# Performance work log

Measured on AMD Instinct MI355X. Metric: run time of the kernel, lower is better.

Reference implementation:

```python
import jax, jax.numpy as jnp
import numpy as np

GRID_SIZE = 5
SPLINE_ORDER = 3
NUM_BASIS = GRID_SIZE + SPLINE_ORDER  # 8


def make_grid():
    # knots: grid_size + 2*spline_order + 1 = 12 points over extended [-1,1]
    h = 2.0 / GRID_SIZE
    return (jnp.arange(-SPLINE_ORDER, GRID_SIZE + SPLINE_ORDER + 1, dtype=jnp.float32) * h - 1.0)[None, :]  # (1, 12)


def b_splines(x, grid):
    # x: (N, in) -> bases: (N, in, NUM_BASIS) via Cox-de Boor recursion
    x = x[..., None]  # (N, in, 1)
    bases = ((x >= grid[:, :-1]) & (x < grid[:, 1:])).astype(x.dtype)
    for p in range(1, SPLINE_ORDER + 1):
        left = (x - grid[:, : -(p + 1)]) / (grid[:, p:-1] - grid[:, : -(p + 1)])
        right = (grid[:, p + 1:] - x) / (grid[:, p + 1:] - grid[:, 1:-p])
        bases = left * bases[..., :-1] + right * bases[..., 1:]
    return bases


def kan_linear(x, base_w, spline_w, scaler, grid):
    # x: (N, in); base_w: (out, in); spline_w: (out, in, G); scaler: (out, in)
    base = jnp.einsum('ni,oi->no', jax.nn.silu(x), base_w)
    bases = b_splines(x, grid)  # (N, in, G)
    spline = jnp.einsum('nig,oig->no', bases, spline_w * scaler[..., None])
    return base + spline


def setup_inputs() -> dict:
    key = jax.random.key(0)
    ks = jax.random.split(key, 7)
    H, L = 768, 2
    hidden = jax.random.normal(ks[0], (32, 512, H), dtype=jnp.float32)
    s = 0.1
    return {
        'hidden': hidden,
        'base_w1': jax.random.normal(ks[1], (H, H), jnp.float32) * s,
        'spline_w1': jax.random.normal(ks[2], (H, H, NUM_BASIS), jnp.float32) * s,
        'scaler1': jax.random.normal(ks[3], (H, H), jnp.float32) * s + 1.0,
        'base_w2': jax.random.normal(ks[4], (L, H), jnp.float32) * s,
        'spline_w2': jax.random.normal(ks[5], (L, H, NUM_BASIS), jnp.float32) * s,
        'scaler2': jax.random.normal(ks[6], (L, H), jnp.float32) * s + 1.0,
    }


def reference(hidden, base_w1, spline_w1, scaler1, base_w2, spline_w2, scaler2):
    grid = make_grid()
    B, S, H = hidden.shape
    x = hidden.reshape(-1, H)  # (N, H)
    x = kan_linear(x, base_w1, spline_w1, scaler1, grid)
    x = jax.nn.gelu(x, approximate=False)  # torch F.gelu default = erf
    out = kan_linear(x, base_w2, spline_w2, scaler2, grid)  # (N, L)
    return out.reshape(B, S, -1).squeeze(-1) if out.shape[-1] == 1 else out.reshape(B, S, -1)
```

## Files before the change

kernel.cpp:

```cpp
#include <hip/hip_runtime.h>
#include <math.h>

#define NROWS 16384
#define H     768
#define KEXP  6912
#define NCHUNK 108
#define NITER 54

typedef __attribute__((ext_vector_type(8))) short  bhalf8;
typedef __attribute__((ext_vector_type(4))) float  floatx4;

__device__ __forceinline__ unsigned short f2bf(float f) {
    unsigned int u = __float_as_uint(f);
    u = (u + 0x7FFFu + ((u >> 16) & 1u)) >> 16;
    return (unsigned short)u;
}
__device__ __forceinline__ float bf2f(unsigned short h) {
    return __uint_as_float(((unsigned int)h) << 16);
}
__device__ __forceinline__ unsigned int pack2(unsigned short a, unsigned short b) {
    return (unsigned int)a | ((unsigned int)b << 16);
}
__device__ __forceinline__ float silu_f(float x) { return x / (1.0f + __expf(-x)); }

__device__ __forceinline__ float gelu_fast(float x) {
    float x3 = x * x * x;
    float y = fmaf(x3, 0.0356774081f, x * 0.7978845608f);
    float e = __expf(2.0f * y);
    float th = 1.0f - 2.0f / (e + 1.0f);
    return 0.5f * x * (1.0f + th);
}

__device__ __forceinline__ void kan_bases(float x, float* __restrict__ b) {
    const float c6 = 0.166666666667f;
    float u  = fmaf(x, 2.5f, 5.5f);
    float fj = floorf(u);
    float t  = u - fj;
    int  j0  = (int)fj;
    float t2 = t * t, t3 = t2 * t;
    float n0 = t3 * c6;
    float n1 = fmaf(t3, -0.5f, fmaf(t2, 0.5f, fmaf(t, 0.5f, c6)));
    float n2 = fmaf(t3, 0.5f, fmaf(t2, -1.0f, 0.666666666667f));
    float omt = 1.0f - t;
    float n3 = omt * omt * omt * c6;
#pragma unroll
    for (int c = 0; c < 8; ++c) {
        int d = j0 - c;
        float v = (d == 0) ? n0 : 0.0f;
        v = (d == 1) ? n1 : v;
        v = (d == 2) ? n2 : v;
        v = (d == 3) ? n3 : v;
        b[c] = v;
    }
}

__global__ __launch_bounds__(256) void prep_expand(
    const float* __restrict__ x, const float* __restrict__ bw,
    const float* __restrict__ sw, const float* __restrict__ sc,
    unsigned short* __restrict__ wp, unsigned short* __restrict__ F)
{
    const int b = blockIdx.x, t = threadIdx.x;
    if (b < 6144) {
        const int e0 = b * 2048 + t;
#pragma unroll
        for (int j = 0; j < 8; ++j) {
            int e = e0 + j * 256;
            int n = e / 768;
            int i = e - n * 768;
            float xv = x[e];
            unsigned short* out = F + (size_t)n * KEXP;
            out[i] = f2bf(silu_f(xv));
            float bb[8];
            kan_bases(xv, bb);
            uint4 pk;
            pk.x = pack2(f2bf(bb[0]), f2bf(bb[1]));
            pk.y = pack2(f2bf(bb[2]), f2bf(bb[3]));
            pk.z = pack2(f2bf(bb[4]), f2bf(bb[5]));
            pk.w = pack2(f2bf(bb[6]), f2bf(bb[7]));
            *(uint4*)(out + H + (size_t)i * 8) = pk;
        }
    } else {
        const int n = b - 6144;
        const float* bwr = bw + (size_t)n * H;
        unsigned short* out = wp + (size_t)n * KEXP;
        if (t < 96) {
            const float4* xp = (const float4*)(bwr + t * 8);
            float4 v0 = xp[0], v1 = xp[1];
            uint4 pk;
            pk.x = pack2(f2bf(v0.x), f2bf(v0.y));
            pk.y = pack2(f2bf(v0.z), f2bf(v0.w));
            pk.z = pack2(f2bf(v1.x), f2bf(v1.y));
            pk.w = pack2(f2bf(v1.z), f2bf(v1.w));
            *(uint4*)(out + t * 8) = pk;
        }
#pragma unroll
        for (int p = 0; p < 3; ++p) {
            int i = t + p * 256;
            float s = sc[(size_t)n * H + i];
            const float4* swp = (const float4*)(sw + ((size_t)n * H + i) * 8);
            float4 w0 = swp[0], w1 = swp[1];
            uint4 pk;
            pk.x = pack2(f2bf(w0.x * s), f2bf(w0.y * s));
            pk.y = pack2(f2bf(w0.z * s), f2bf(w0.w * s));
            pk.z = pack2(f2bf(w1.x * s), f2bf(w1.y * s));
            pk.w = pack2(f2bf(w1.z * s), f2bf(w1.w * s));
            *(uint4*)(out + H + (size_t)i * 8) = pk;
        }
    }
}


#define AS1 __attribute__((address_space(1)))
#define AS3 __attribute__((address_space(3)))

#define DSR(D, A, O) asm volatile("ds_read_b128 %0, %1 offset:" #O : "=v"(D) : "v"(A) : "memory")
#define LDA0(O) do{ DSR(fA0[0],avA[0],O); DSR(fA0[1],avA[1],O); DSR(fA0[2],avA[2],O); DSR(fA0[3],avA[3],O); \
                    DSR(fA0[4],avA[4],O); DSR(fA0[5],avA[5],O); DSR(fA0[6],avA[6],O); DSR(fA0[7],avA[7],O); }while(0)
#define LDA1(O) do{ DSR(fA1[0],avA[0],O); DSR(fA1[1],avA[1],O); DSR(fA1[2],avA[2],O); DSR(fA1[3],avA[3],O); \
                    DSR(fA1[4],avA[4],O); DSR(fA1[5],avA[5],O); DSR(fA1[6],avA[6],O); DSR(fA1[7],avA[7],O); }while(0)
#define LDB(O)  do{ DSR(fB[0],avB[0],O); DSR(fB[1],avB[1],O); }while(0)

#define MM0(QN) do{ \
    _Pragma("unroll") \
    for (int kk = 0; kk < 2; ++kk) \
        _Pragma("unroll") \
        for (int im = 0; im < 4; ++im) \
            acc0[QN][im] = __builtin_amdgcn_mfma_f32_16x16x32_bf16( \
                fA0[im*2+kk], fB[kk], acc0[QN][im], 0, 0, 0); \
}while(0)
#define MM1(QN) do{ \
    _Pragma("unroll") \
    for (int kk = 0; kk < 2; ++kk) \
        _Pragma("unroll") \
        for (int im = 0; im < 4; ++im) \
            acc1[QN][im] = __builtin_amdgcn_mfma_f32_16x16x32_bf16( \
                fA1[im*2+kk], fB[kk], acc1[QN][im], 0, 0, 0); \
}while(0)

#define STG_A(BF,HH,KS) do{ \
    __builtin_amdgcn_global_load_lds((const AS1 void*)(pA##HH[0] + (size_t)(KS)*64), \
        (AS3 void*)&sA[BF][HH][wb8], 16, 0, 0); \
    __builtin_amdgcn_global_load_lds((const AS1 void*)(pA##HH[1] + (size_t)(KS)*64), \
        (AS3 void*)&sA[BF][HH][4096 + wb8], 16, 0, 0); \
}while(0)
#define STG_B(BF,QN,KS) \
    __builtin_amdgcn_global_load_lds((const AS1 void*)(pB[QN] + (size_t)(KS)*64), \
        (AS3 void*)&sB[BF][QN][wb8], 16, 0, 0)

#define PH_MID do{ __builtin_amdgcn_s_barrier(); \
    asm volatile("s_waitcnt lgkmcnt(0)" ::: "memory"); \
    __builtin_amdgcn_sched_barrier(0); \
    __builtin_amdgcn_s_setprio(1); }while(0)
#define PH_END do{ __builtin_amdgcn_s_setprio(0); \
    __builtin_amdgcn_sched_barrier(0); \
    __builtin_amdgcn_s_barrier(); }while(0)
#define PH_END_VMN(N) do{ __builtin_amdgcn_s_setprio(0); \
    __builtin_amdgcn_sched_barrier(0); \
    asm volatile("s_waitcnt vmcnt(" #N ")" ::: "memory"); \
    __builtin_amdgcn_s_barrier(); }while(0)

__global__ __launch_bounds__(512, 2) void kan1_gemm(
    const unsigned short* __restrict__ F, const unsigned short* __restrict__ wp,
    unsigned short* __restrict__ l1)
{
    __shared__ __align__(16) unsigned short sA[2][2][8192];
    __shared__ __align__(16) unsigned short sB[2][3][4096];

    const int b = blockIdx.x;
    const int s = b >> 3;
    const int rowT = (b & 7) * 8 + (s >> 2);
    const int colT = s & 3;
    const int rowBase = rowT * 256, colBase = colT * 192;

    const int t = threadIdx.x;
    const int lane = t & 63;
    const int quad = lane >> 4, lm = lane & 15, p7 = lane & 7;
    const int wv = t >> 6, wr = wv & 1, wc = wv >> 1;

    const int rr = t >> 3;
    const int slotx = (t & 7) ^ (rr & 7);
    const int wb8 = (t & 448) * 8;

    const unsigned short* pA0[2]; const unsigned short* pA1[2];
    const unsigned short* pB[3];
#pragma unroll
    for (int p = 0; p < 2; ++p) {
        pA0[p] = F + (size_t)(rowBase +       p*64 + rr) * KEXP + slotx*8;
        pA1[p] = F + (size_t)(rowBase + 128 + p*64 + rr) * KEXP + slotx*8;
    }
#pragma unroll
    for (int q = 0; q < 3; ++q)
        pB[q] = wp + (size_t)(colBase + q*64 + rr) * KEXP + slotx*8;

    unsigned int avA[8], avB[2];
    {
        unsigned int aB = (unsigned int)(size_t)(AS3 unsigned short*)&sA[0][0][0];
        unsigned int bB = (unsigned int)(size_t)(AS3 unsigned short*)&sB[0][0][0];
#pragma unroll
        for (int im = 0; im < 4; ++im)
#pragma unroll
            for (int kk = 0; kk < 2; ++kk)
                avA[im*2+kk] = aB + (unsigned)(((wr*64 + im*16 + lm)*64 + (((kk*4+quad)^p7)*8)) * 2);
#pragma unroll
        for (int kk = 0; kk < 2; ++kk)
            avB[kk] = bB + (unsigned)(((wc*16 + lm)*64 + (((kk*4+quad)^p7)*8)) * 2);
    }

    floatx4 acc0[3][4] = {};
    floatx4 acc1[3][4] = {};
    bhalf8 fA0[8], fA1[8], fB[2];

    STG_A(0,0,0); STG_A(0,1,0); STG_B(0,0,0); STG_B(0,1,0); STG_B(0,2,0);
    STG_A(1,0,1); STG_A(1,1,1); STG_B(1,0,1); STG_B(1,1,1);
    asm volatile("s_waitcnt vmcnt(8)" ::: "memory");
    __builtin_amdgcn_s_barrier();

#pragma unroll 1
    for (int i = 0; i < NITER; ++i) {
        const int k1 = 2*i + 1;
        const int k2 = (2*i + 2 > 107) ? 107 : 2*i + 2;
        const int k3 = (2*i + 3 > 107) ? 107 : 2*i + 3;
        LDA0(0);     LDB(0);     STG_B(1,2,k1);               PH_MID; MM0(0);         PH_END_VMN(10);
        LDA1(16384);             STG_A(0,0,k2);               PH_MID; MM1(0);         PH_END_VMN(10);
        LDB(8192);               STG_A(0,1,k2);               PH_MID; MM1(1); MM0(1); PH_END_VMN(11);
        LDB(16384);              STG_B(0,0,k2); STG_B(0,1,k2);PH_MID; MM0(2); MM1(2); PH_END_VMN(8);
        LDA0(32768); LDB(24576); STG_B(0,2,k2);               PH_MID; MM0(0);         PH_END;
        LDA1(49152);             STG_A(1,0,k3);               PH_MID; MM1(0);         PH_END_VMN(10);
        LDB(32768);              STG_A(1,1,k3);               PH_MID; MM1(1); MM0(1); PH_END_VMN(11);
        LDB(40960);              STG_B(1,0,k3); STG_B(1,1,k3);PH_MID; MM0(2); MM1(2); PH_END_VMN(8);
    }

#pragma unroll
    for (int qn = 0; qn < 3; ++qn)
#pragma unroll
    for (int im = 0; im < 4; ++im) {
        const int col = colBase + qn*64 + wc*16 + lm;
        {
            const int row0 = rowBase + wr*64 + im*16 + quad*4;
#pragma unroll
            for (int rg = 0; rg < 4; ++rg)
                l1[(size_t)(row0 + rg) * H + col] = f2bf(acc0[qn][im][rg]);
        }
        {
            const int row0 = rowBase + 128 + wr*64 + im*16 + quad*4;
#pragma unroll
            for (int rg = 0; rg < 4; ++rg)
                l1[(size_t)(row0 + rg) * H + col] = f2bf(acc1[qn][im][rg]);
        }
    }
}

__global__ __launch_bounds__(256) void kan2_kernel(
    const unsigned short* __restrict__ l1, const float* __restrict__ bw,
    const float* __restrict__ sw, const float* __restrict__ sc,
    float* __restrict__ out)
{
    const int lane = threadIdx.x & 63;
    const int wv = threadIdx.x >> 6;
    const int n = blockIdx.x * 4 + wv;
    float a0 = 0.f, a1 = 0.f;
#pragma unroll
    for (int ii = 0; ii < H / 64; ++ii) {
        int i = lane + ii * 64;
        float h = bf2f(l1[(size_t)n * H + i]);
        float u = gelu_fast(h);
        float f0 = silu_f(u);
        float bb[8];
        kan_bases(u, bb);
        float bw0 = bw[i], bw1 = bw[H + i];
        float s0 = sc[i], s1 = sc[H + i];
        const float4* q0 = (const float4*)(sw + (size_t)i * 8);
        const float4* q1 = (const float4*)(sw + (size_t)(H + i) * 8);
        float4 w00 = q0[0], w01 = q0[1];
        float4 w10 = q1[0], w11 = q1[1];
        float t0 = bb[0]*w00.x + bb[1]*w00.y + bb[2]*w00.z + bb[3]*w00.w
                 + bb[4]*w01.x + bb[5]*w01.y + bb[6]*w01.z + bb[7]*w01.w;
        float t1 = bb[0]*w10.x + bb[1]*w10.y + bb[2]*w10.z + bb[3]*w10.w
                 + bb[4]*w11.x + bb[5]*w11.y + bb[6]*w11.z + bb[7]*w11.w;
        a0 += f0 * bw0 + s0 * t0;
        a1 += f0 * bw1 + s1 * t1;
    }
#pragma unroll
    for (int off = 32; off > 0; off >>= 1) {
        a0 += __shfl_down(a0, off, 64);
        a1 += __shfl_down(a1, off, 64);
    }
    if (lane == 0) {
        out[(size_t)n * 2 + 0] = a0;
        out[(size_t)n * 2 + 1] = a1;
    }
}

extern "C" void kernel_launch(void* const* d_in, const int* in_sizes, int n_in,
                              void* d_out, int out_size, void* d_ws, size_t ws_size,
                              hipStream_t stream) {
    const float* hidden = (const float*)d_in[0];
    const float* bw1    = (const float*)d_in[1];
    const float* sw1    = (const float*)d_in[2];
    const float* sc1    = (const float*)d_in[3];
    const float* bw2    = (const float*)d_in[4];
    const float* sw2    = (const float*)d_in[5];
    const float* sc2    = (const float*)d_in[6];
    float* out = (float*)d_out;

    const size_t l1_elems = (size_t)NROWS * H;
    const size_t wp_elems = (size_t)H * KEXP;
    unsigned short* l1 = (unsigned short*)d_ws;
    unsigned short* wp = l1 + l1_elems;
    unsigned short* F  = wp + wp_elems;

    prep_expand<<<6144 + H, 256, 0, stream>>>(hidden, bw1, sw1, sc1, wp, F);
    kan1_gemm<<<256, 512, 0, stream>>>(F, wp, l1);
    kan2_kernel<<<NROWS / 4, 256, 0, stream>>>(l1, bw2, sw2, sc2, out);
}
```

Baseline: 332.5 us.

## Fuse second KAN layer into GEMM epilogue with atomic row reductions

```diff
diff --git a/kernel.cpp b/kernel.cpp
--- a/kernel.cpp
+++ b/kernel.cpp
@@ -159,9 +159,48 @@
     asm volatile("s_waitcnt vmcnt(" #N ")" ::: "memory"); \
     __builtin_amdgcn_s_barrier(); }while(0)
 
-__global__ __launch_bounds__(512, 2) void kan1_gemm(
+#define EPI_HALF(ACC, QMOFF) do{ \
+    _Pragma("unroll") \
+    for (int im = 0; im < 4; ++im) { \
+        _Pragma("unroll") \
+        for (int rg = 0; rg < 4; ++rg) { \
+            float p0 = 0.f, p1 = 0.f; \
+            _Pragma("unroll") \
+            for (int qn = 0; qn < 3; ++qn) { \
+                float v = ACC[qn][im][rg]; \
+                float u = gelu_fast(v); \
+                float f0v = silu_f(u); \
+                float bb[8]; \
+                kan_bases(u, bb); \
+                float t0 = bb[0]*wsw[qn][0][0].x + bb[1]*wsw[qn][0][0].y \
+                         + bb[2]*wsw[qn][0][0].z + bb[3]*wsw[qn][0][0].w \
+                         + bb[4]*wsw[qn][0][1].x + bb[5]*wsw[qn][0][1].y \
+                         + bb[6]*wsw[qn][0][1].z + bb[7]*wsw[qn][0][1].w; \
+                float t1 = bb[0]*wsw[qn][1][0].x + bb[1]*wsw[qn][1][0].y \
+                         + bb[2]*wsw[qn][1][0].z + bb[3]*wsw[qn][1][0].w \
+                         + bb[4]*wsw[qn][1][1].x + bb[5]*wsw[qn][1][1].y \
+                         + bb[6]*wsw[qn][1][1].z + bb[7]*wsw[qn][1][1].w; \
+                p0 += fmaf(f0v, wbw[qn][0], wsc[qn][0] * t0); \
+                p1 += fmaf(f0v, wbw[qn][1], wsc[qn][1] * t1); \
+            } \
+            _Pragma("unroll") \
+            for (int off = 8; off > 0; off >>= 1) { \
+                p0 += __shfl_xor(p0, off, 64); \
+                p1 += __shfl_xor(p1, off, 64); \
+            } \
+            if (lm == 0) { \
+                int row = rowBase + (QMOFF) + wr*64 + im*16 + quad*4 + rg; \
+                atomicAdd(&outp[(size_t)row * 2 + 0], p0); \
+                atomicAdd(&outp[(size_t)row * 2 + 1], p1); \
+            } \
+        } \
+    } \
+}while(0)
+
+__global__ __launch_bounds__(512, 2) void kan1_fused(
     const unsigned short* __restrict__ F, const unsigned short* __restrict__ wp,
-    unsigned short* __restrict__ l1)
+    const float* __restrict__ bw2, const float* __restrict__ sw2,
+    const float* __restrict__ sc2, float* __restrict__ outp)
 {
     __shared__ __align__(16) unsigned short sA[2][2][8192];
     __shared__ __align__(16) unsigned short sB[2][3][4096];
@@ -230,65 +269,20 @@
         LDB(40960);              STG_B(1,0,k3); STG_B(1,1,k3);PH_MID; MM0(2); MM1(2); PH_END_VMN(8);
     }
 
-#pragma unroll
-    for (int qn = 0; qn < 3; ++qn)
-#pragma unroll
-    for (int im = 0; im < 4; ++im) {
-        const int col = colBase + qn*64 + wc*16 + lm;
-        {
-            const int row0 = rowBase + wr*64 + im*16 + quad*4;
-#pragma unroll
-            for (int rg = 0; rg < 4; ++rg)
-                l1[(size_t)(row0 + rg) * H + col] = f2bf(acc0[qn][im][rg]);
-        }
-        {
-            const int row0 = rowBase + 128 + wr*64 + im*16 + quad*4;
-#pragma unroll
-            for (int rg = 0; rg < 4; ++rg)
-                l1[(size_t)(row0 + rg) * H + col] = f2bf(acc1[qn][im][rg]);
-        }
-    }
-}
-
-__global__ __launch_bounds__(256) void kan2_kernel(
-    const unsigned short* __restrict__ l1, const float* __restrict__ bw,
-    const float* __restrict__ sw, const float* __restrict__ sc,
-    float* __restrict__ out)
-{
-    const int lane = threadIdx.x & 63;
-    const int wv = threadIdx.x >> 6;
-    const int n = blockIdx.x * 4 + wv;
-    float a0 = 0.f, a1 = 0.f;
-#pragma unroll
-    for (int ii = 0; ii < H / 64; ++ii) {
-        int i = lane + ii * 64;
-        float h = bf2f(l1[(size_t)n * H + i]);
-        float u = gelu_fast(h);
-        float f0 = silu_f(u);
-        float bb[8];
-        kan_bases(u, bb);
-        float bw0 = bw[i], bw1 = bw[H + i];
-        float s0 = sc[i], s1 = sc[H + i];
-        const float4* q0 = (const float4*)(sw + (size_t)i * 8);
-        const float4* q1 = (const float4*)(sw + (size_t)(H + i) * 8);
-        float4 w00 = q0[0], w01 = q0[1];
-        float4 w10 = q1[0], w11 = q1[1];
-        float t0 = bb[0]*w00.x + bb[1]*w00.y + bb[2]*w00.z + bb[3]*w00.w
-                 + bb[4]*w01.x + bb[5]*w01.y + bb[6]*w01.z + bb[7]*w01.w;
-        float t1 = bb[0]*w10.x + bb[1]*w10.y + bb[2]*w10.z + bb[3]*w10.w
-                 + bb[4]*w11.x + bb[5]*w11.y + bb[6]*w11.z + bb[7]*w11.w;
-        a0 += f0 * bw0 + s0 * t0;
-        a1 += f0 * bw1 + s1 * t1;
-    }
-#pragma unroll
-    for (int off = 32; off > 0; off >>= 1) {
-        a0 += __shfl_down(a0, off, 64);
-        a1 += __shfl_down(a1, off, 64);
-    }
-    if (lane == 0) {
-        out[(size_t)n * 2 + 0] = a0;
-        out[(size_t)n * 2 + 1] = a1;
-    }
+    float  wbw[3][2], wsc[3][2];
+    float4 wsw[3][2][2];
+#pragma unroll
+    for (int qn = 0; qn < 3; ++qn) {
+        const int i = colBase + qn*64 + wc*16 + lm;
+        wbw[qn][0] = bw2[i];      wbw[qn][1] = bw2[H + i];
+        wsc[qn][0] = sc2[i];      wsc[qn][1] = sc2[H + i];
+        const float4* q0 = (const float4*)(sw2 + (size_t)i * 8);
+        const float4* q1 = (const float4*)(sw2 + (size_t)(H + i) * 8);
+        wsw[qn][0][0] = q0[0];    wsw[qn][0][1] = q0[1];
+        wsw[qn][1][0] = q1[0];    wsw[qn][1][1] = q1[1];
+    }
+    EPI_HALF(acc0, 0);
+    EPI_HALF(acc1, 128);
 }
 
 extern "C" void kernel_launch(void* const* d_in, const int* in_sizes, int n_in,
@@ -303,13 +297,11 @@
     const float* sc2    = (const float*)d_in[6];
     float* out = (float*)d_out;
 
-    const size_t l1_elems = (size_t)NROWS * H;
     const size_t wp_elems = (size_t)H * KEXP;
-    unsigned short* l1 = (unsigned short*)d_ws;
-    unsigned short* wp = l1 + l1_elems;
+    unsigned short* wp = (unsigned short*)d_ws;
     unsigned short* F  = wp + wp_elems;
 
+    hipMemsetAsync(d_out, 0, (size_t)out_size, stream);
     prep_expand<<<6144 + H, 256, 0, stream>>>(hidden, bw1, sw1, sc1, wp, F);
-    kan1_gemm<<<256, 512, 0, stream>>>(F, wp, l1);
-    kan2_kernel<<<NROWS / 4, 256, 0, stream>>>(l1, bw2, sw2, sc2, out);
-}
+    kan1_fused<<<256, 512, 0, stream>>>(F, wp, bw2, sw2, sc2, out);
+}
```

Result: faster. 324.6 us (-2.4%).

## Fuse second KAN layer into GEMM epilogue with atomic row reduction

Applied to the files above, without the earlier changes.

```diff
diff --git a/kernel.cpp b/kernel.cpp
--- a/kernel.cpp
+++ b/kernel.cpp
@@ -9,6 +9,7 @@
 
 typedef __attribute__((ext_vector_type(8))) short  bhalf8;
 typedef __attribute__((ext_vector_type(4))) float  floatx4;
+typedef __attribute__((ext_vector_type(4))) unsigned int uintx4;
 
 __device__ __forceinline__ unsigned short f2bf(float f) {
     unsigned int u = __float_as_uint(f);
@@ -21,13 +22,15 @@
 __device__ __forceinline__ unsigned int pack2(unsigned short a, unsigned short b) {
     return (unsigned int)a | ((unsigned int)b << 16);
 }
-__device__ __forceinline__ float silu_f(float x) { return x / (1.0f + __expf(-x)); }
+__device__ __forceinline__ float silu_f(float x) {
+    return x * __builtin_amdgcn_rcpf(1.0f + __expf(-x));
+}
 
 __device__ __forceinline__ float gelu_fast(float x) {
     float x3 = x * x * x;
     float y = fmaf(x3, 0.0356774081f, x * 0.7978845608f);
     float e = __expf(2.0f * y);
-    float th = 1.0f - 2.0f / (e + 1.0f);
+    float th = 1.0f - 2.0f * __builtin_amdgcn_rcpf(e + 1.0f);
     return 0.5f * x * (1.0f + th);
 }
 
@@ -69,15 +72,15 @@
             int i = e - n * 768;
             float xv = x[e];
             unsigned short* out = F + (size_t)n * KEXP;
-            out[i] = f2bf(silu_f(xv));
+            __builtin_nontemporal_store(f2bf(silu_f(xv)), out + i);
             float bb[8];
             kan_bases(xv, bb);
-            uint4 pk;
+            uintx4 pk;
             pk.x = pack2(f2bf(bb[0]), f2bf(bb[1]));
             pk.y = pack2(f2bf(bb[2]), f2bf(bb[3]));
             pk.z = pack2(f2bf(bb[4]), f2bf(bb[5]));
             pk.w = pack2(f2bf(bb[6]), f2bf(bb[7]));
-            *(uint4*)(out + H + (size_t)i * 8) = pk;
+            __builtin_nontemporal_store(pk, (uintx4*)(out + H + (size_t)i * 8));
         }
     } else {
         const int n = b - 6144;
@@ -86,12 +89,12 @@
         if (t < 96) {
             const float4* xp = (const float4*)(bwr + t * 8);
             float4 v0 = xp[0], v1 = xp[1];
-            uint4 pk;
+            uintx4 pk;
             pk.x = pack2(f2bf(v0.x), f2bf(v0.y));
             pk.y = pack2(f2bf(v0.z), f2bf(v0.w));
             pk.z = pack2(f2bf(v1.x), f2bf(v1.y));
             pk.w = pack2(f2bf(v1.z), f2bf(v1.w));
-            *(uint4*)(out + t * 8) = pk;
+            __builtin_nontemporal_store(pk, (uintx4*)(out + t * 8));
         }
 #pragma unroll
         for (int p = 0; p < 3; ++p) {
@@ -99,12 +102,12 @@
             float s = sc[(size_t)n * H + i];
             const float4* swp = (const float4*)(sw + ((size_t)n * H + i) * 8);
             float4 w0 = swp[0], w1 = swp[1];
-            uint4 pk;
+            uintx4 pk;
             pk.x = pack2(f2bf(w0.x * s), f2bf(w0.y * s));
             pk.y = pack2(f2bf(w0.z * s), f2bf(w0.w * s));
             pk.z = pack2(f2bf(w1.x * s), f2bf(w1.y * s));
             pk.w = pack2(f2bf(w1.z * s), f2bf(w1.w * s));
-            *(uint4*)(out + H + (size_t)i * 8) = pk;
+            __builtin_nontemporal_store(pk, (uintx4*)(out + H + (size_t)i * 8));
         }
     }
 }
@@ -159,9 +162,10 @@
     asm volatile("s_waitcnt vmcnt(" #N ")" ::: "memory"); \
     __builtin_amdgcn_s_barrier(); }while(0)
 
-__global__ __launch_bounds__(512, 2) void kan1_gemm(
+__global__ __launch_bounds__(512, 2) void kan1_fused(
     const unsigned short* __restrict__ F, const unsigned short* __restrict__ wp,
-    unsigned short* __restrict__ l1)
+    const float* __restrict__ bw2, const float* __restrict__ sw2,
+    const float* __restrict__ sc2, float* __restrict__ outp)
 {
     __shared__ __align__(16) unsigned short sA[2][2][8192];
     __shared__ __align__(16) unsigned short sB[2][3][4096];
@@ -230,64 +234,68 @@
         LDB(40960);              STG_B(1,0,k3); STG_B(1,1,k3);PH_MID; MM0(2); MM1(2); PH_END_VMN(8);
     }
 
-#pragma unroll
-    for (int qn = 0; qn < 3; ++qn)
-#pragma unroll
-    for (int im = 0; im < 4; ++im) {
-        const int col = colBase + qn*64 + wc*16 + lm;
-        {
-            const int row0 = rowBase + wr*64 + im*16 + quad*4;
-#pragma unroll
-            for (int rg = 0; rg < 4; ++rg)
-                l1[(size_t)(row0 + rg) * H + col] = f2bf(acc0[qn][im][rg]);
-        }
-        {
-            const int row0 = rowBase + 128 + wr*64 + im*16 + quad*4;
-#pragma unroll
-            for (int rg = 0; rg < 4; ++rg)
-                l1[(size_t)(row0 + rg) * H + col] = f2bf(acc1[qn][im][rg]);
-        }
-    }
-}
-
-__global__ __launch_bounds__(256) void kan2_kernel(
-    const unsigned short* __restrict__ l1, const float* __restrict__ bw,
-    const float* __restrict__ sw, const float* __restrict__ sc,
-    float* __restrict__ out)
-{
-    const int lane = threadIdx.x & 63;
-    const int wv = threadIdx.x >> 6;
-    const int n = blockIdx.x * 4 + wv;
-    float a0 = 0.f, a1 = 0.f;
-#pragma unroll
-    for (int ii = 0; ii < H / 64; ++ii) {
-        int i = lane + ii * 64;
-        float h = bf2f(l1[(size_t)n * H + i]);
-        float u = gelu_fast(h);
-        float f0 = silu_f(u);
-        float bb[8];
-        kan_bases(u, bb);
-        float bw0 = bw[i], bw1 = bw[H + i];
-        float s0 = sc[i], s1 = sc[H + i];
-        const float4* q0 = (const float4*)(sw + (size_t)i * 8);
-        const float4* q1 = (const float4*)(sw + (size_t)(H + i) * 8);
-        float4 w00 = q0[0], w01 = q0[1];
-        float4 w10 = q1[0], w11 = q1[1];
-        float t0 = bb[0]*w00.x + bb[1]*w00.y + bb[2]*w00.z + bb[3]*w00.w
-                 + bb[4]*w01.x + bb[5]*w01.y + bb[6]*w01.z + bb[7]*w01.w;
-        float t1 = bb[0]*w10.x + bb[1]*w10.y + bb[2]*w10.z + bb[3]*w10.w
-                 + bb[4]*w11.x + bb[5]*w11.y + bb[6]*w11.z + bb[7]*w11.w;
-        a0 += f0 * bw0 + s0 * t0;
-        a1 += f0 * bw1 + s1 * t1;
-    }
-#pragma unroll
-    for (int off = 32; off > 0; off >>= 1) {
-        a0 += __shfl_down(a0, off, 64);
-        a1 += __shfl_down(a1, off, 64);
-    }
-    if (lane == 0) {
-        out[(size_t)n * 2 + 0] = a0;
-        out[(size_t)n * 2 + 1] = a1;
+    float p00[4][4] = {}, p01[4][4] = {};
+    float p10[4][4] = {}, p11[4][4] = {};
+#pragma unroll
+    for (int qn = 0; qn < 3; ++qn) {
+        const int i = colBase + qn*64 + wc*16 + lm;
+        const float bwa = bw2[i], bwb = bw2[H + i];
+        const float sca = sc2[i], scb = sc2[H + i];
+        const float4* q0 = (const float4*)(sw2 + (size_t)i * 8);
+        const float4* q1 = (const float4*)(sw2 + (size_t)(H + i) * 8);
+        const float4 wa0 = q0[0], wa1 = q0[1];
+        const float4 wb0 = q1[0], wb1 = q1[1];
+#pragma unroll
+        for (int im = 0; im < 4; ++im)
+#pragma unroll
+        for (int rg = 0; rg < 4; ++rg) {
+            {
+                float u = gelu_fast(acc0[qn][im][rg]);
+                float f0v = silu_f(u);
+                float bb[8];
+                kan_bases(u, bb);
+                float t0 = bb[0]*wa0.x + bb[1]*wa0.y + bb[2]*wa0.z + bb[3]*wa0.w
+                         + bb[4]*wa1.x + bb[5]*wa1.y + bb[6]*wa1.z + bb[7]*wa1.w;
+                float t1 = bb[0]*wb0.x + bb[1]*wb0.y + bb[2]*wb0.z + bb[3]*wb0.w
+                         + bb[4]*wb1.x + bb[5]*wb1.y + bb[6]*wb1.z + bb[7]*wb1.w;
+                p00[im][rg] += fmaf(f0v, bwa, sca * t0);
+                p01[im][rg] += fmaf(f0v, bwb, scb * t1);
+            }
+            {
+                float u = gelu_fast(acc1[qn][im][rg]);
+                float f0v = silu_f(u);
+                float bb[8];
+                kan_bases(u, bb);
+                float t0 = bb[0]*wa0.x + bb[1]*wa0.y + bb[2]*wa0.z + bb[3]*wa0.w
+                         + bb[4]*wa1.x + bb[5]*wa1.y + bb[6]*wa1.z + bb[7]*wa1.w;
+                float t1 = bb[0]*wb0.x + bb[1]*wb0.y + bb[2]*wb0.z + bb[3]*wb0.w
+                         + bb[4]*wb1.x + bb[5]*wb1.y + bb[6]*wb1.z + bb[7]*wb1.w;
+                p10[im][rg] += fmaf(f0v, bwa, sca * t0);
+                p11[im][rg] += fmaf(f0v, bwb, scb * t1);
+            }
+        }
+    }
+#pragma unroll
+    for (int im = 0; im < 4; ++im)
+#pragma unroll
+    for (int rg = 0; rg < 4; ++rg) {
+        float a0 = p00[im][rg], a1 = p01[im][rg];
+        float c0 = p10[im][rg], c1 = p11[im][rg];
+#pragma unroll
+        for (int off = 8; off > 0; off >>= 1) {
+            a0 += __shfl_xor(a0, off, 64);
+            a1 += __shfl_xor(a1, off, 64);
+            c0 += __shfl_xor(c0, off, 64);
+            c1 += __shfl_xor(c1, off, 64);
+        }
+        if (lm == 0) {
+            const int row0 = rowBase + wr*64 + im*16 + quad*4 + rg;
+            atomicAdd(&outp[(size_t)row0 * 2 + 0], a0);
+            atomicAdd(&outp[(size_t)row0 * 2 + 1], a1);
+            const int row1 = row0 + 128;
+            atomicAdd(&outp[(size_t)row1 * 2 + 0], c0);
+            atomicAdd(&outp[(size_t)row1 * 2 + 1], c1);
+        }
     }
 }
 
@@ -303,13 +311,11 @@
     const float* sc2    = (const float*)d_in[6];
     float* out = (float*)d_out;
 
-    const size_t l1_elems = (size_t)NROWS * H;
     const size_t wp_elems = (size_t)H * KEXP;
-    unsigned short* l1 = (unsigned short*)d_ws;
-    unsigned short* wp = l1 + l1_elems;
+    unsigned short* wp = (unsigned short*)d_ws;
     unsigned short* F  = wp + wp_elems;
 
+    hipMemsetAsync(d_out, 0, (size_t)out_size, stream);
     prep_expand<<<6144 + H, 256, 0, stream>>>(hidden, bw1, sw1, sc1, wp, F);
-    kan1_gemm<<<256, 512, 0, stream>>>(F, wp, l1);
-    kan2_kernel<<<NROWS / 4, 256, 0, stream>>>(l1, bw2, sw2, sc2, out);
-}
+    kan1_fused<<<256, 512, 0, stream>>>(F, wp, bw2, sw2, sc2, out);
+}
```

New measurement: 308.2 us. 7.3% less time.
